# Kernel tuning notes

Measured on AMD Instinct MI355X. Metric: run time of the kernel, lower is better.

Reference implementation:

```python
import jax, jax.numpy as jnp
import numpy as np

GROUPS = 32
EPS = 1e-6
C = 512
HEADS = 8
B, N, K = 1, 2048, 128


def group_norm(x, w, b):
    # x: [B, C, N]
    Bx, Cx, Nx = x.shape
    xg = x.reshape(Bx, GROUPS, Cx // GROUPS, Nx)
    mu = xg.mean(axis=(2, 3), keepdims=True)
    var = xg.var(axis=(2, 3), keepdims=True)
    xn = ((xg - mu) / jnp.sqrt(var + EPS)).reshape(Bx, Cx, Nx)
    return xn * w[:, None] + b[:, None]


def conv1x1(h, w, b):
    # 1x1 Conv1d == per-position linear: w [out, in], h [B, in, N]
    return jnp.einsum('oc,bcn->bon', w, h) + b[:, None]


def setup_inputs() -> dict:
    key = jax.random.key(0)
    ks = jax.random.split(key, 8)
    x = jax.random.normal(ks[0], (B, C, N), dtype=jnp.float32)
    valid_indices_mask = jax.random.randint(ks[1], (N, K), 0, 2, dtype=jnp.int32)
    attendable_indices = jax.random.randint(ks[2], (N, K), 0, N, dtype=jnp.int32)
    s = 0.05
    return {
        'x': x,
        'valid_indices_mask': valid_indices_mask,
        'attendable_indices': attendable_indices,
        'gn_w': jnp.ones((C,), jnp.float32),
        'gn_b': jnp.zeros((C,), jnp.float32),
        'wq': jax.random.normal(ks[3], (C, C), jnp.float32) * s,
        'bq': jnp.zeros((C,), jnp.float32),
        'wk': jax.random.normal(ks[4], (C, C), jnp.float32) * s,
        'bk': jnp.zeros((C,), jnp.float32),
        'wv': jax.random.normal(ks[5], (C, C), jnp.float32) * s,
        'bv': jnp.zeros((C,), jnp.float32),
        'wp': jax.random.normal(ks[6], (C, C), jnp.float32) * s,
        'bp': jnp.zeros((C,), jnp.float32),
    }


def reference(x, valid_indices_mask, attendable_indices, gn_w, gn_b,
              wq, bq, wk, bk, wv, bv, wp, bp):
    b, c, n = x.shape
    d = c // HEADS
    h_ = group_norm(x, gn_w, gn_b)
    q = conv1x1(h_, wq, bq).reshape(b, HEADS, d, n)
    k = conv1x1(h_, wk, bk).reshape(b, HEADS, d, n)
    v = conv1x1(h_, wv, bv).reshape(b, HEADS, d, n)

    # gather per-query attendable keys/values: [b,h,n,d] indexed by [nq,K] -> [b,h,nq,K,d]
    kt = jnp.swapaxes(k, -1, -2)
    vt = jnp.swapaxes(v, -1, -2)
    ak = kt[:, :, attendable_indices]  # [b,h,nq,K,d]
    av = vt[:, :, attendable_indices]

    # beta = 1, no 1/sqrt(d) scaling in the sparse path (faithful to source)
    weights = jnp.einsum('bhqkd,bhdq->bhqk', ak, q)
    weights = jnp.where(valid_indices_mask[None, None] == 0, -jnp.inf, weights)
    weights = jax.nn.softmax(weights, axis=-1)

    o = jnp.einsum('bhqk,bhqkd->bhqd', weights, av)
    # permute(0,3,1,2).reshape(b,c,n): channel layout is d-major then head (as in source)
    o = jnp.transpose(o, (0, 3, 1, 2)).reshape(b, c, n)
    o = conv1x1(o, wp, bp)
    return x + o
```

## Files before the change

### kernel.cpp

```cpp
#include <hip/hip_runtime.h>
#include <hip/hip_bf16.h>
#include <math.h>

#define NPOS 2048
#define CH   512
#define KATT 128
#define NHEAD 8

typedef __attribute__((ext_vector_type(8))) short short8;
typedef __attribute__((ext_vector_type(4))) float f32x4;

static __device__ __forceinline__ ushort f2bf(float f) {
  union { float f; unsigned u; } v; v.f = f;
  unsigned r = (v.u + 0x7FFFu + ((v.u >> 16) & 1u)) >> 16;
  return (ushort)r;
}
static __device__ __forceinline__ float bf2f(ushort u) {
  union { unsigned u; float f; } v; v.u = ((unsigned)u) << 16;
  return v.f;
}

static __device__ __forceinline__ void gl16(const void* g, void* l) {
  __builtin_amdgcn_global_load_lds(
      (const __attribute__((address_space(1))) unsigned int*)(uintptr_t)g,
      (__attribute__((address_space(3))) unsigned int*)(uintptr_t)l, 16, 0, 0);
}

__global__ __launch_bounds__(256) void prep_k(const float* __restrict__ x,
    const float* __restrict__ wq, const float* __restrict__ wk,
    const float* __restrict__ wv, const float* __restrict__ wp,
    const float* __restrict__ bq, const float* __restrict__ bk,
    const float* __restrict__ bv, float* __restrict__ part,
    ushort* __restrict__ wqkv, ushort* __restrict__ wppb,
    float* __restrict__ bqkv) {
  const int bid = blockIdx.x;
  if (bid < 256) {
    const int b = bid;
    const float* xp = x + (b >> 3) * 32768 + (b & 7) * 4096;
    float s = 0.f, ss = 0.f;
    for (int i = threadIdx.x; i < 4096; i += 256) {
      float v = xp[i];
      s += v;
      ss += v * v;
    }
    __shared__ float rs[256], rq[256];
    rs[threadIdx.x] = s;
    rq[threadIdx.x] = ss;
    __syncthreads();
    for (int off = 128; off > 0; off >>= 1) {
      if (threadIdx.x < (unsigned)off) {
        rs[threadIdx.x] += rs[threadIdx.x + off];
        rq[threadIdx.x] += rq[threadIdx.x + off];
      }
      __syncthreads();
    }
    if (threadIdx.x == 0) {
      part[b * 2] = rs[0];
      part[b * 2 + 1] = rq[0];
    }
  } else if (bid < 1024) {
    const int wb = bid - 256;
    const int m = wb >> 8;
    const float* src = m == 0 ? wq : (m == 1 ? wk : wv);
    const int i = (wb & 255) * 1024 + threadIdx.x * 4;
    const float4 v = *(const float4*)(src + i);
    uint2 p;
    p.x = (unsigned)f2bf(v.x) | ((unsigned)f2bf(v.y) << 16);
    p.y = (unsigned)f2bf(v.z) | ((unsigned)f2bf(v.w) << 16);
    *(uint2*)(wqkv + m * 262144 + i) = p;
  } else if (bid < 1152) {
    __shared__ float lds[2048];
    const int co0 = (bid - 1024) * 4;
    for (int t = threadIdx.x; t < 2048; t += 256) lds[t] = wp[co0 * 512 + t];
    __syncthreads();
    ushort o8[8];
#pragma unroll
    for (int e = 0; e < 8; ++e) {
      const int jj = threadIdx.x * 8 + e;
      const int col = jj >> 9;
      const int sl = jj & 511;
      o8[e] = f2bf(lds[col * 512 + (sl & 63) * 8 + (sl >> 6)]);
    }
    *(uint4*)(wppb + co0 * 512 + threadIdx.x * 8) = *(uint4*)o8;
  } else {
    for (int i = threadIdx.x; i < 1536; i += 256)
      bqkv[i] = i < 512 ? bq[i] : (i < 1024 ? bk[i - 512] : bv[i - 1024]);
  }
}

__global__ __launch_bounds__(256) void gn2_k(const float* __restrict__ x,
    const float* __restrict__ part, const float* __restrict__ gw,
    const float* __restrict__ gb, ushort* __restrict__ ht) {
  const int g = blockIdx.x >> 4;
  const int chunk = blockIdx.x & 15;
  float s = 0.f, ss = 0.f;
#pragma unroll
  for (int o = 0; o < 8; ++o) {
    s += part[(g * 8 + o) * 2];
    ss += part[(g * 8 + o) * 2 + 1];
  }
  const float inv_n = 1.f / 32768.f;
  const float mu = s * inv_n;
  const float var = ss * inv_n - mu * mu;
  const float rstd = rsqrtf(var + 1e-6f);

  const int half = threadIdx.x >> 7;
  const int pos = chunk * 128 + (threadIdx.x & 127);
  unsigned pk[4];
#pragma unroll
  for (int c2 = 0; c2 < 4; ++c2) {
    unsigned p = 0;
#pragma unroll
    for (int e = 0; e < 2; ++e) {
      const int cc = half * 8 + c2 * 2 + e;
      const int ch = g * 16 + cc;
      const float a = gw[ch] * rstd;
      const float v = x[ch * NPOS + pos] * a + (gb[ch] - mu * a);
      p |= ((unsigned)f2bf(v)) << (16 * e);
    }
    pk[c2] = p;
  }
  *(uint4*)(ht + pos * CH + g * 16 + half * 8) = make_uint4(pk[0], pk[1], pk[2], pk[3]);
}

template<int TM, int WN, int MODE>
__global__ __launch_bounds__(256) void mm_k(const ushort* __restrict__ A,
    const ushort* __restrict__ Bm, const float* __restrict__ bias,
    const float* __restrict__ resid, float* __restrict__ outF,
    ushort* __restrict__ outV) {
  constexpr int WM = 4 / WN;
  constexpr int FM = TM / (WM * 16);
  constexpr int FN = 64 / (WN * 16);
  __shared__ ushort As[TM * 64];
  __shared__ ushort Bs[64 * 64];
  const int mBase = blockIdx.x * TM;
  const int nBase = blockIdx.y * 64;
  const int tid = threadIdx.x;
  const int l = tid & 63;
  const int w = tid >> 6;
  const int wm = w / WN, wn = w % WN;
  const int sub8 = l >> 3;
  const int c16 = (l & 7) << 4;
  f32x4 acc[FM][FN] = {};

  for (int k0 = 0; k0 < 512; k0 += 64) {
#pragma unroll
    for (int c = 0; c < TM / 32; ++c) {
      const int r0 = w * (TM / 4) + c * 8;
      const int row = r0 + sub8;
      const int sc = c16 ^ ((row & 7) << 4);
      gl16(A + (mBase + row) * 512 + k0 + (sc >> 1), (char*)As + r0 * 128);
    }
#pragma unroll
    for (int c = 0; c < 2; ++c) {
      const int r0 = w * 16 + c * 8;
      const int row = r0 + sub8;
      const int sc = c16 ^ ((row & 7) << 4);
      gl16(Bm + (nBase + row) * 512 + k0 + (sc >> 1), (char*)Bs + r0 * 128);
    }
    __syncthreads();
#pragma unroll
    for (int ks = 0; ks < 2; ++ks) {
      const int kb = ks * 64 + ((l >> 4) << 4);
      short8 afr[FM], bfr[FN];
#pragma unroll
      for (int fm = 0; fm < FM; ++fm) {
        const int ra = wm * (FM * 16) + fm * 16 + (l & 15);
        afr[fm] = *(const short8*)((const char*)As + ra * 128 + (kb ^ ((ra & 7) << 4)));
      }
#pragma unroll
      for (int fn = 0; fn < FN; ++fn) {
        const int rb = wn * (FN * 16) + fn * 16 + (l & 15);
        bfr[fn] = *(const short8*)((const char*)Bs + rb * 128 + (kb ^ ((rb & 7) << 4)));
      }
#pragma unroll
      for (int fm = 0; fm < FM; ++fm)
#pragma unroll
        for (int fn = 0; fn < FN; ++fn)
          acc[fm][fn] = __builtin_amdgcn_mfma_f32_16x16x32_bf16(afr[fm], bfr[fn], acc[fm][fn], 0, 0, 0);
    }
    __syncthreads();
  }

#pragma unroll
  for (int fm = 0; fm < FM; ++fm)
#pragma unroll
    for (int fn = 0; fn < FN; ++fn) {
      const int col = nBase + wn * (FN * 16) + fn * 16 + (l & 15);
#pragma unroll
      for (int r = 0; r < 4; ++r) {
        const int rowm = mBase + wm * (FM * 16) + fm * 16 + ((l >> 4) << 2) + r;
        if (MODE == 0) {
          const float v = acc[fm][fn][r] + bias[col];
          if (col < 1024) {
            outF[(col >> 9) * (NPOS * CH) + rowm * CH + (col & 511)] = v;
          } else {
            outV[rowm * CH + (col & 511)] = f2bf(v);
          }
        } else {
          const int off = rowm * NPOS + col;
          outF[off] = acc[fm][fn][r] + bias[rowm] + resid[off];
        }
      }
    }
}

__global__ __launch_bounds__(256) void attn_k(const float* __restrict__ qt,
    const float* __restrict__ kt, const ushort* __restrict__ vtb,
    const int* __restrict__ aidx, const int* __restrict__ vmask,
    ushort* __restrict__ ot) {
  __shared__ int ils[4][KATT];
  __shared__ float scs[4][KATT];
  __shared__ float prs[4][2 * KATT];
  const int w = threadIdx.x >> 6;
  const int lane = threadIdx.x & 63;
  const int p = blockIdx.x * 4 + w;
  const int hd = p & 7;
  const int qpos = p >> 3;
  const int quad = lane >> 2;
  const int sub = lane & 3;
  int* ils_w = ils[w];
  float* scs_w = scs[w];
  float* prs_w = prs[w];

  const float* qb = qt + qpos * CH + hd * 64;
  float4 qv[4];
#pragma unroll
  for (int t = 0; t < 4; ++t) qv[t] = *(const float4*)(qb + t * 16 + sub * 4);

  const int i0 = qpos * KATT + lane;
  const int idx0 = aidx[i0];
  const int idx1 = aidx[i0 + 64];
  const int m0 = vmask[i0];
  const int m1 = vmask[i0 + 64];

  const unsigned long long b0 = __ballot(m0 != 0);
  const unsigned long long b1 = __ballot(m1 != 0);
  const int nv0 = __popcll(b0);
  const int nv = nv0 + __popcll(b1);
  const unsigned long long low = (1ull << lane) - 1ull;
  ils_w[lane] = 0;
  ils_w[lane + 64] = 0;
  if (m0) ils_w[__popcll(b0 & low)] = idx0;
  if (m1) ils_w[nv0 + __popcll(b1 & low)] = idx1;

  const int P = (nv + 15) >> 4;
  for (int p8 = 0; p8 < P; p8 += 2) {
    const int t0 = p8 * 16 + quad;
    const int t1 = t0 + 16;
    const bool has1 = (p8 + 1) < P;
    const int ki0 = ils_w[t0];
    const int ki1 = has1 ? ils_w[t1] : 0;
    const float* kr0 = kt + ki0 * CH + hd * 64;
    const float* kr1 = kt + ki1 * CH + hd * 64;
    float4 kc0[4], kc1[4];
#pragma unroll
    for (int tt = 0; tt < 4; ++tt) kc0[tt] = *(const float4*)(kr0 + tt * 16 + sub * 4);
#pragma unroll
    for (int tt = 0; tt < 4; ++tt) kc1[tt] = *(const float4*)(kr1 + tt * 16 + sub * 4);
    float s0 = 0.f, s1 = 0.f;
#pragma unroll
    for (int tt = 0; tt < 4; ++tt) {
      s0 += kc0[tt].x * qv[tt].x + kc0[tt].y * qv[tt].y + kc0[tt].z * qv[tt].z + kc0[tt].w * qv[tt].w;
      s1 += kc1[tt].x * qv[tt].x + kc1[tt].y * qv[tt].y + kc1[tt].z * qv[tt].z + kc1[tt].w * qv[tt].w;
    }
    s0 += __shfl_xor(s0, 1); s0 += __shfl_xor(s0, 2);
    s1 += __shfl_xor(s1, 1); s1 += __shfl_xor(s1, 2);
    if (sub == 0 && t0 < nv) scs_w[t0] = s0;
    if (sub == 0 && has1 && t1 < nv) scs_w[t1] = s1;
  }

  float s0 = (lane < nv) ? scs_w[lane] : -INFINITY;
  float s1 = (lane + 64 < nv) ? scs_w[lane + 64] : -INFINITY;
  float mx = fmaxf(s0, s1);
#pragma unroll
  for (int off = 32; off > 0; off >>= 1) mx = fmaxf(mx, __shfl_xor(mx, off));
  const float e0 = __expf(s0 - mx);
  const float e1 = __expf(s1 - mx);
  float lsum = (lane < nv ? e0 : 0.f) + (lane + 64 < nv ? e1 : 0.f);
#pragma unroll
  for (int off = 32; off > 0; off >>= 1) lsum += __shfl_xor(lsum, off);
  const float inv = 1.f / lsum;

  if (lane < nv) {
    prs_w[2 * lane] = e0 * inv;
    prs_w[2 * lane + 1] = __int_as_float(ils_w[lane]);
  }
  if (lane + 64 < nv) {
    prs_w[2 * (lane + 64)] = e1 * inv;
    prs_w[2 * (lane + 64) + 1] = __int_as_float(ils_w[lane + 64]);
  }

  const ushort* vb = vtb + hd * 64 + lane;
  float o = 0.f;
  int kk = 0;
  for (; kk + 8 <= nv; kk += 8) {
    const float4 c0 = *(const float4*)&prs_w[2 * kk];
    const float4 c1 = *(const float4*)&prs_w[2 * kk + 4];
    const float4 c2 = *(const float4*)&prs_w[2 * kk + 8];
    const float4 c3 = *(const float4*)&prs_w[2 * kk + 12];
    float vv[8];
    vv[0] = bf2f(vb[__float_as_int(c0.y) * CH]);
    vv[1] = bf2f(vb[__float_as_int(c0.w) * CH]);
    vv[2] = bf2f(vb[__float_as_int(c1.y) * CH]);
    vv[3] = bf2f(vb[__float_as_int(c1.w) * CH]);
    vv[4] = bf2f(vb[__float_as_int(c2.y) * CH]);
    vv[5] = bf2f(vb[__float_as_int(c2.w) * CH]);
    vv[6] = bf2f(vb[__float_as_int(c3.y) * CH]);
    vv[7] = bf2f(vb[__float_as_int(c3.w) * CH]);
    o += c0.x * vv[0] + c0.z * vv[1] + c1.x * vv[2] + c1.z * vv[3] +
         c2.x * vv[4] + c2.z * vv[5] + c3.x * vv[6] + c3.z * vv[7];
  }
  for (; kk < nv; ++kk) {
    const float2 c = *(const float2*)&prs_w[2 * kk];
    o += c.x * bf2f(vb[__float_as_int(c.y) * CH]);
  }
  ot[qpos * CH + hd * 64 + lane] = f2bf(o);
}

extern "C" void kernel_launch(void* const* d_in, const int* in_sizes, int n_in,
                              void* d_out, int out_size, void* d_ws, size_t ws_size,
                              hipStream_t stream) {
  const float* x    = (const float*)d_in[0];
  const int* vmask  = (const int*)d_in[1];
  const int* aidx   = (const int*)d_in[2];
  const float* gnw  = (const float*)d_in[3];
  const float* gnb  = (const float*)d_in[4];
  const float* wq   = (const float*)d_in[5];
  const float* bq   = (const float*)d_in[6];
  const float* wk   = (const float*)d_in[7];
  const float* bk   = (const float*)d_in[8];
  const float* wv   = (const float*)d_in[9];
  const float* bv   = (const float*)d_in[10];
  const float* wp   = (const float*)d_in[11];
  const float* bp   = (const float*)d_in[12];
  float* out = (float*)d_out;

  char* ws = (char*)d_ws;
  ushort* ht    = (ushort*)(ws);
  float*  qt    = (float*)(ws + (2u  << 20));
  float*  kt    = (float*)(ws + (6u  << 20));
  ushort* vtb   = (ushort*)(ws + (10u << 20));
  ushort* ot    = (ushort*)(ws + (14u << 20));
  ushort* wqkv  = (ushort*)(ws + (16u << 20));
  ushort* wppb  = (ushort*)(ws + (17u << 20) + (512u << 10));
  float*  bqkv  = (float*)(ws + (18u << 20));
  float*  part  = (float*)(ws + (18u << 20) + (32u << 10));

  prep_k<<<1153, 256, 0, stream>>>(x, wq, wk, wv, wp, bq, bk, bv,
                                   part, wqkv, wppb, bqkv);
  gn2_k<<<512, 256, 0, stream>>>(x, part, gnw, gnb, ht);

  mm_k<64, 2, 0><<<dim3(NPOS / 64, 1536 / 64), 256, 0, stream>>>(
      ht, wqkv, bqkv, nullptr, qt, vtb);

  attn_k<<<(NPOS * NHEAD) / 4, 256, 0, stream>>>(qt, kt, vtb, aidx, vmask, ot);

  mm_k<32, 4, 1><<<dim3(CH / 32, NPOS / 64), 256, 0, stream>>>(
      wppb, ot, bp, x, out, nullptr);
}
```

Baseline: 130.3 us.

## Double-buffer LDS tiles in GEMM kernel and shrink QKV tile height

Adds a second LDS buffer for the A and B tiles so the async global-to-LDS load of the next K-slice is issued before the MFMA work on the current slice, with one barrier per iteration. This aims to hide global load latency behind compute. The QKV projection GEMM also switches from a 64-row to a 32-row M tile, doubling the grid size for better CU occupancy at the cost of less B-tile reuse. LDS use per block doubles.

```diff
diff --git a/kernel.cpp b/kernel.cpp
--- a/kernel.cpp
+++ b/kernel.cpp
@@ -131,8 +131,8 @@
   constexpr int WM = 4 / WN;
   constexpr int FM = TM / (WM * 16);
   constexpr int FN = 64 / (WN * 16);
-  __shared__ ushort As[TM * 64];
-  __shared__ ushort Bs[64 * 64];
+  __shared__ ushort As[2][TM * 64];
+  __shared__ ushort Bs[2][64 * 64];
   const int mBase = blockIdx.x * TM;
   const int nBase = blockIdx.y * 64;
   const int tid = threadIdx.x;
@@ -143,22 +143,31 @@
   const int c16 = (l & 7) << 4;
   f32x4 acc[FM][FN] = {};
 
-  for (int k0 = 0; k0 < 512; k0 += 64) {
-#pragma unroll
-    for (int c = 0; c < TM / 32; ++c) {
-      const int r0 = w * (TM / 4) + c * 8;
-      const int row = r0 + sub8;
-      const int sc = c16 ^ ((row & 7) << 4);
-      gl16(A + (mBase + row) * 512 + k0 + (sc >> 1), (char*)As + r0 * 128);
-    }
-#pragma unroll
-    for (int c = 0; c < 2; ++c) {
-      const int r0 = w * 16 + c * 8;
-      const int row = r0 + sub8;
-      const int sc = c16 ^ ((row & 7) << 4);
-      gl16(Bm + (nBase + row) * 512 + k0 + (sc >> 1), (char*)Bs + r0 * 128);
-    }
-    __syncthreads();
+#define MM_STAGE(buf, kk0)                                                  \
+  {                                                                         \
+    _Pragma("unroll")                                                       \
+    for (int c = 0; c < TM / 32; ++c) {                                     \
+      const int r0 = w * (TM / 4) + c * 8;                                  \
+      const int row = r0 + sub8;                                            \
+      const int sc = c16 ^ ((row & 7) << 4);                                \
+      gl16(A + (mBase + row) * 512 + (kk0) + (sc >> 1),                     \
+           (char*)As[buf] + r0 * 128);                                      \
+    }                                                                       \
+    _Pragma("unroll")                                                       \
+    for (int c = 0; c < 2; ++c) {                                           \
+      const int r0 = w * 16 + c * 8;                                        \
+      const int row = r0 + sub8;                                            \
+      const int sc = c16 ^ ((row & 7) << 4);                                \
+      gl16(Bm + (nBase + row) * 512 + (kk0) + (sc >> 1),                    \
+           (char*)Bs[buf] + r0 * 128);                                      \
+    }                                                                       \
+  }
+
+  MM_STAGE(0, 0);
+  __syncthreads();
+  int cur = 0;
+  for (int t = 0; t < 8; ++t) {
+    if (t < 7) MM_STAGE(cur ^ 1, (t + 1) * 64);
 #pragma unroll
     for (int ks = 0; ks < 2; ++ks) {
       const int kb = ks * 64 + ((l >> 4) << 4);
@@ -166,12 +175,12 @@
 #pragma unroll
       for (int fm = 0; fm < FM; ++fm) {
         const int ra = wm * (FM * 16) + fm * 16 + (l & 15);
-        afr[fm] = *(const short8*)((const char*)As + ra * 128 + (kb ^ ((ra & 7) << 4)));
+        afr[fm] = *(const short8*)((const char*)As[cur] + ra * 128 + (kb ^ ((ra & 7) << 4)));
       }
 #pragma unroll
       for (int fn = 0; fn < FN; ++fn) {
         const int rb = wn * (FN * 16) + fn * 16 + (l & 15);
-        bfr[fn] = *(const short8*)((const char*)Bs + rb * 128 + (kb ^ ((rb & 7) << 4)));
+        bfr[fn] = *(const short8*)((const char*)Bs[cur] + rb * 128 + (kb ^ ((rb & 7) << 4)));
       }
 #pragma unroll
       for (int fm = 0; fm < FM; ++fm)
@@ -180,7 +189,9 @@
           acc[fm][fn] = __builtin_amdgcn_mfma_f32_16x16x32_bf16(afr[fm], bfr[fn], acc[fm][fn], 0, 0, 0);
     }
     __syncthreads();
-  }
+    cur ^= 1;
+  }
+#undef MM_STAGE
 
 #pragma unroll
   for (int fm = 0; fm < FM; ++fm)
@@ -351,7 +362,7 @@
                                    part, wqkv, wppb, bqkv);
   gn2_k<<<512, 256, 0, stream>>>(x, part, gnw, gnb, ht);
 
-  mm_k<64, 2, 0><<<dim3(NPOS / 64, 1536 / 64), 256, 0, stream>>>(
+  mm_k<32, 2, 0><<<dim3(NPOS / 32, 1536 / 64), 256, 0, stream>>>(
       ht, wqkv, bqkv, nullptr, qt, vtb);
 
   attn_k<<<(NPOS * NHEAD) / 4, 256, 0, stream>>>(qt, kt, vtb, aidx, vmask, ot);
```

Measured after the change: 129.6 us. About the same (-0.6%).
